# Performance work log

Hardware: AMD Instinct MI355X
Metric: run time of the kernel (lower is better)

## Reference

```python
import jax, jax.numpy as jnp
import numpy as np

N = 50000
E = 800000
IN_C = 256
NHID = 32
HEADS = 4
OUT_C = 64
HID = NHID * HEADS  # 128
SLOPE = 0.2


def setup_inputs() -> dict:
    key = jax.random.key(0)
    ks = jax.random.split(key, 16)
    s = lambda *d: 1.0 / np.sqrt(d[0])
    inp = {
        "x": jax.random.normal(ks[0], (N, IN_C), dtype=jnp.float32),
        "edge_index": jax.random.randint(ks[1], (2, E), 0, N, dtype=jnp.int64),
        # conv1: GATConv(IN_C, NHID, heads=HEADS, concat=True)
        "W1": jax.random.normal(ks[2], (IN_C, HEADS * NHID), dtype=jnp.float32) * s(IN_C),
        "att_src1": jax.random.normal(ks[3], (HEADS, NHID), dtype=jnp.float32) * s(NHID),
        "att_dst1": jax.random.normal(ks[4], (HEADS, NHID), dtype=jnp.float32) * s(NHID),
        "b1": jnp.zeros((HEADS * NHID,), dtype=jnp.float32),
        # conv2: GATConv(HID, OUT_C, heads=1, concat=False)
        "W2": jax.random.normal(ks[5], (HID, OUT_C), dtype=jnp.float32) * s(HID),
        "att_src2": jax.random.normal(ks[6], (1, OUT_C), dtype=jnp.float32) * s(OUT_C),
        "att_dst2": jax.random.normal(ks[7], (1, OUT_C), dtype=jnp.float32) * s(OUT_C),
        "b2": jnp.zeros((OUT_C,), dtype=jnp.float32),
        # res1: Linear(IN_C, HID)
        "res1_w": jax.random.normal(ks[8], (IN_C, HID), dtype=jnp.float32) * s(IN_C),
        "res1_b": jnp.zeros((HID,), dtype=jnp.float32),
        # fc: Linear(HID, OUT_C)
        "fc_w": jax.random.normal(ks[9], (HID, OUT_C), dtype=jnp.float32) * s(HID),
        "fc_b": jnp.zeros((OUT_C,), dtype=jnp.float32),
    }
    return inp


def leaky_relu(x, slope=SLOPE):
    return jnp.where(x >= 0, x, slope * x)


def gat_conv(x, edge_index, W, att_src, att_dst, bias, heads, out_c, concat):
    """PyG GATConv with default add_self_loops=True, negative_slope=0.2."""
    n = x.shape[0]
    loop = jnp.arange(n, dtype=edge_index.dtype)
    src = jnp.concatenate([edge_index[0], loop])  # [E+N]
    dst = jnp.concatenate([edge_index[1], loop])
    h = (x @ W).reshape(n, heads, out_c)          # [N,H,C]
    a_src = (h * att_src[None]).sum(-1)           # [N,H]
    a_dst = (h * att_dst[None]).sum(-1)
    alpha = leaky_relu(a_src[src] + a_dst[dst])   # [E+N,H]
    # segment softmax over destination nodes (every node has a self loop)
    amax = jax.ops.segment_max(alpha, dst, num_segments=n)
    expa = jnp.exp(alpha - amax[dst])
    denom = jax.ops.segment_sum(expa, dst, num_segments=n)
    alpha = expa / (denom[dst] + 1e-16)
    msg = alpha[:, :, None] * h[src]              # [E+N,H,C] irregular gather
    out = jax.ops.segment_sum(msg, dst, num_segments=n)  # scatter-add
    if concat:
        out = out.reshape(n, heads * out_c)
    else:
        out = out.mean(axis=1)
    return out + bias


def reference(x, edge_index, W1, att_src1, att_dst1, b1, W2, att_src2, att_dst2, b2,
              res1_w, res1_b, fc_w, fc_b):
    x_res = x @ res1_w + res1_b
    h = gat_conv(x, edge_index, W1, att_src1, att_dst1, b1, HEADS, NHID, True) + x_res
    h_res = h @ fc_w + fc_b
    h = leaky_relu(h)
    z = gat_conv(h, edge_index, W2, att_src2, att_dst2, b2, 1, OUT_C, False) + h_res
    z = leaky_relu(z)
    return z
```

## Files before the change

### kernel.cpp

```cpp
#include <hip/hip_runtime.h>

typedef __attribute__((ext_vector_type(8))) short short8;
typedef __attribute__((ext_vector_type(4))) float f32x4;

constexpr int BCAP = 4096;

__device__ __forceinline__ ushort rne_bf16(float f) {
  uint u = __float_as_uint(f);
  uint r = (u + 0x7FFFu + ((u >> 16) & 1u)) >> 16;
  return (ushort)r;
}
__device__ __forceinline__ float bf16_lo(uint pair) { return __uint_as_float(pair << 16); }
__device__ __forceinline__ float bf16_hi(uint pair) { return __uint_as_float(pair & 0xffff0000u); }
__device__ __forceinline__ float bf1(ushort v) { return __uint_as_float((uint)v << 16); }
__device__ __forceinline__ float lrelu(float a) { return a >= 0.f ? a : 0.2f * a; }

__device__ __forceinline__ uint lrelu_pair(uint pair) {
  float lo = lrelu(bf16_lo(pair));
  float hi = lrelu(bf16_hi(pair));
  return (uint)rne_bf16(lo) | ((uint)rne_bf16(hi) << 16);
}
__device__ __forceinline__ float4 lrelu_bf8(float4 v) {
  uint4 u = *(uint4*)&v;
  u.x = lrelu_pair(u.x); u.y = lrelu_pair(u.y);
  u.z = lrelu_pair(u.z); u.w = lrelu_pair(u.w);
  return *(float4*)&u;
}

__global__ __launch_bounds__(256) void prep_all_k(
    const float* __restrict__ x, ushort* __restrict__ x_bf, long nitems,
    const int* __restrict__ ei, int E, int nEB,
    int* __restrict__ bcnt, uint2* __restrict__ tmp, int nbuck,
    const float* __restrict__ W1, const float* __restrict__ res1_w,
    const float* __restrict__ fc_w, const float* __restrict__ W2,
    ushort* __restrict__ Wt1, ushort* __restrict__ fcT, ushort* __restrict__ W2T)
{
  __shared__ int lcnt[400];
  __shared__ int gbase[400];
  const int tid = threadIdx.x, bid = blockIdx.x;
  const long gstride = (long)gridDim.x * 256;
  const long g0 = (long)bid * 256 + tid;

  for (long it = g0; it < nitems; it += gstride) {
    long i = it * 8;
    float4 a = *(const float4*)&x[i];
    float4 b = *(const float4*)&x[i + 4];
    ushort o[8] = {rne_bf16(a.x), rne_bf16(a.y), rne_bf16(a.z), rne_bf16(a.w),
                   rne_bf16(b.x), rne_bf16(b.y), rne_bf16(b.z), rne_bf16(b.w)};
    *(uint4*)&x_bf[i] = *(const uint4*)o;
  }

  if (bid < nEB) {
    for (int i = tid; i < nbuck; i += 256) lcnt[i] = 0;
    __syncthreads();
    const int ebase = bid * 4096;
    int srcs[16], dsts[16], rk[16];
#pragma unroll
    for (int i = 0; i < 16; ++i) {
      int e = ebase + i * 256 + tid;
      if (e < E) {
        srcs[i] = ei[e];
        dsts[i] = ei[E + e];
        rk[i] = atomicAdd(&lcnt[dsts[i] >> 7], 1);
      } else dsts[i] = -1;
    }
    __syncthreads();
    for (int b = tid; b < nbuck; b += 256)
      gbase[b] = lcnt[b] ? atomicAdd(&bcnt[b], lcnt[b]) : 0;
    __syncthreads();
#pragma unroll
    for (int i = 0; i < 16; ++i) {
      if (dsts[i] >= 0) {
        int b = dsts[i] >> 7;
        tmp[(size_t)b * BCAP + gbase[b] + rk[i]] = make_uint2((uint)srcs[i], (uint)dsts[i]);
      }
    }
  }

  for (long gi = g0; gi < 81920; gi += gstride) {
    const float* src; ushort* dst; int K, NO; long local;
    if (gi < 32768)            { src = W1;     dst = Wt1;          K = 256; NO = 128; local = gi; }
    else if (gi < 65536)       { src = res1_w; dst = Wt1 + 32768;  K = 256; NO = 128; local = gi - 32768; }
    else if (gi < 65536+8192)  { src = fc_w;   dst = fcT;          K = 128; NO = 64;  local = gi - 65536; }
    else                       { src = W2;     dst = W2T;          K = 128; NO = 64;  local = gi - 65536 - 8192; }
    int n = (int)(local / K), k = (int)(local % K);
    dst[local] = rne_bf16(src[(size_t)k * NO + n]);
  }
}

__global__ __launch_bounds__(512) void scan_buckets_k(const int* __restrict__ bcnt,
                                                      int* __restrict__ bbase,
                                                      int* __restrict__ offp,
                                                      int nbuck, int N) {
  __shared__ int sh[512];
  int tid = threadIdx.x;
  int v = (tid < nbuck) ? bcnt[tid] : 0;
  sh[tid] = v;
  __syncthreads();
  for (int o = 1; o < 512; o <<= 1) {
    int t = (tid >= o) ? sh[tid - o] : 0;
    __syncthreads();
    sh[tid] += t;
    __syncthreads();
  }
  if (tid < nbuck) bbase[tid] = sh[tid] - v;
  if (tid == nbuck - 1) { bbase[nbuck] = sh[tid]; offp[N] = sh[tid]; }
}

__global__ __launch_bounds__(512) void gemm1_k(
    const ushort* __restrict__ x_bf, const ushort* __restrict__ Wt1,
    const float* __restrict__ res1_b,
    const float* __restrict__ att_s1, const float* __restrict__ att_d1,
    ushort* __restrict__ h1bf, ushort* __restrict__ xresbf,
    float* __restrict__ a_s, float* __restrict__ a_d,
    const uint2* __restrict__ tmp, const int* __restrict__ bcnt,
    const int* __restrict__ bbase, int* __restrict__ offp,
    int* __restrict__ csr, int nbuck, int M)
{
  constexpr int LDA = 72;
  __shared__ ushort smem[64 * LDA + 256 * LDA];
  const int bid = blockIdx.x, tid = threadIdx.x;
  ushort* As = smem;
  ushort* Bs = smem + 64 * LDA;
  const int w = tid >> 6, l = tid & 63;
  const int wr = w >> 2, wc = w & 3;
  const int l15 = l & 15, lg = l >> 4;
  const int row0 = bid * 64;
  const int srow = tid >> 3, sch = tid & 7;

  int gra = row0 + srow; if (gra >= M) gra = M - 1;
  const ushort* Ap = x_bf + (size_t)gra * 256 + sch * 8;
  const ushort* Bp = Wt1 + (size_t)srow * 256 + sch * 8;

  f32x4 acc[2][4] = {};
  float4 raC, rbC0, rbC1, rbC2, rbC3, raN, rbN0, rbN1, rbN2, rbN3;
  raC  = *(const float4*)(Ap);
  rbC0 = *(const float4*)(Bp);
  rbC1 = *(const float4*)(Bp + 64 * 256);
  rbC2 = *(const float4*)(Bp + 128 * 256);
  rbC3 = *(const float4*)(Bp + 192 * 256);

#pragma unroll
  for (int kt = 0; kt < 4; ++kt) {
    __syncthreads();
    *(float4*)&As[srow * LDA + sch * 8] = raC;
    *(float4*)&Bs[(0 * 64 + srow) * LDA + sch * 8] = rbC0;
    *(float4*)&Bs[(1 * 64 + srow) * LDA + sch * 8] = rbC1;
    *(float4*)&Bs[(2 * 64 + srow) * LDA + sch * 8] = rbC2;
    *(float4*)&Bs[(3 * 64 + srow) * LDA + sch * 8] = rbC3;
    __syncthreads();
    if (kt < 3) {
      int k1 = (kt + 1) * 64;
      raN  = *(const float4*)(Ap + k1);
      rbN0 = *(const float4*)(Bp + k1);
      rbN1 = *(const float4*)(Bp + 64 * 256 + k1);
      rbN2 = *(const float4*)(Bp + 128 * 256 + k1);
      rbN3 = *(const float4*)(Bp + 192 * 256 + k1);
    }
    short8 aF[2][2], bF[4][2];
#pragma unroll
    for (int m = 0; m < 2; ++m)
#pragma unroll
      for (int kk = 0; kk < 2; ++kk)
        aF[m][kk] = *(const short8*)&As[(wr * 32 + m * 16 + l15) * LDA + kk * 32 + lg * 8];
#pragma unroll
    for (int n = 0; n < 4; ++n)
#pragma unroll
      for (int kk = 0; kk < 2; ++kk)
        bF[n][kk] = *(const short8*)&Bs[(wc * 64 + n * 16 + l15) * LDA + kk * 32 + lg * 8];
#pragma unroll
    for (int m = 0; m < 2; ++m)
#pragma unroll
      for (int n = 0; n < 4; ++n)
#pragma unroll
        for (int kk = 0; kk < 2; ++kk)
          acc[m][n] = __builtin_amdgcn_mfma_f32_16x16x32_bf16(aF[m][kk], bF[n][kk], acc[m][n], 0, 0, 0);
    raC = raN; rbC0 = rbN0; rbC1 = rbN1; rbC2 = rbN2; rbC3 = rbN3;
  }
  __syncthreads();

  ushort* Cs = smem;
#pragma unroll
  for (int m = 0; m < 2; ++m)
#pragma unroll
    for (int n = 0; n < 4; ++n)
#pragma unroll
      for (int j = 0; j < 4; ++j) {
        int rl = wr * 32 + m * 16 + lg * 4 + j;
        int col = wc * 64 + n * 16 + l15;
        float v = acc[m][n][j] + (col >= 128 ? res1_b[col - 128] : 0.f);
        Cs[rl * 256 + col] = rne_bf16(v);
      }
  __syncthreads();

  {
    int r = tid >> 3, s = tid & 7, h = s >> 1;
    int gr = row0 + r;
    float ps = 0.f, pd = 0.f;
#pragma unroll
    for (int i = 0; i < 16; ++i) {
      int col = s * 16 + i;
      float v = bf1(Cs[r * 256 + col]);
      ps += v * att_s1[h * 32 + (col & 31)];
      pd += v * att_d1[h * 32 + (col & 31)];
    }
    ps += __shfl_xor(ps, 1, 64);
    pd += __shfl_xor(pd, 1, 64);
    if (!(s & 1) && gr < M) { a_s[gr * 4 + h] = ps; a_d[gr * 4 + h] = pd; }
  }

#pragma unroll
  for (int idx = tid; idx < 2048; idx += 512) {
    int row = idx >> 5, c16 = idx & 31;
    int gr = row0 + row;
    if (gr < M) {
      uint4 v = *(const uint4*)&Cs[row * 256 + c16 * 8];
      if (c16 < 16) *(uint4*)&h1bf[(size_t)gr * 128 + c16 * 8] = v;
      else          *(uint4*)&xresbf[(size_t)gr * 128 + (c16 - 16) * 8] = v;
    }
  }

  if (bid < nbuck) {
    __syncthreads();
    int* lcnt = (int*)smem;
    int* excl = lcnt + 128;
    const int vbase = bid * 128;
    const int nloc = ((vbase + 128 < M) ? 128 : M - vbase);
    const int cntb = bcnt[bid];
    const int bbase0 = bbase[bid];
    const uint2* bt = tmp + (size_t)bid * BCAP;
    if (tid < 128) lcnt[tid] = 0;
    __syncthreads();
    for (int e = tid; e < cntb; e += 512)
      atomicAdd(&lcnt[(int)bt[e].y - vbase], 1);
    __syncthreads();
    if (tid < 128) {
      int v = lcnt[tid];
      int sc = v;
#pragma unroll
      for (int o = 1; o < 64; o <<= 1) {
        int t = __shfl_up(sc, o, 64);
        if ((tid & 63) >= o) sc += t;
      }
      excl[tid] = sc - v;
    }
    __syncthreads();
    if (tid >= 64 && tid < 128) excl[tid] += excl[63] + lcnt[63];
    __syncthreads();
    if (tid < nloc) offp[vbase + tid] = bbase0 + excl[tid];
    if (tid < 128) lcnt[tid] = 0;
    __syncthreads();
    for (int e = tid; e < cntb; e += 512) {
      uint2 t = bt[e];
      int li = (int)t.y - vbase;
      int r = atomicAdd(&lcnt[li], 1);
      csr[bbase0 + excl[li] + r] = (int)t.x;
    }
  }
}

__global__ __launch_bounds__(512) void gemm2_k(
    const ushort* __restrict__ hpre,
    const ushort* __restrict__ fcT,
    const float* __restrict__ fc_b,
    const float* __restrict__ att_s2, const float* __restrict__ att_d2,
    ushort* __restrict__ hresb, ushort* __restrict__ h2bf,
    float* __restrict__ a_s, float* __restrict__ a_d, int M)
{
  constexpr int LDA = 72;
  __shared__ ushort smem[64 * LDA + 64 * LDA];
  const int tid = threadIdx.x, y = blockIdx.y;
  const ushort* B = fcT + (size_t)y * 64 * 128;
  ushort* out = y ? h2bf : hresb;
  const int row0 = blockIdx.x * 64;
  ushort* As = smem;
  ushort* Bs = smem + 64 * LDA;
  const int w = tid >> 6, l = tid & 63;
  const int wr = w >> 1, wc = w & 1;
  const int l15 = l & 15, lg = l >> 4;
  const int srow = tid >> 3, sch = tid & 7;

  int gra = row0 + srow; if (gra >= M) gra = M - 1;
  const ushort* Ap = hpre + (size_t)gra * 128 + sch * 8;
  const ushort* Bp = B + (size_t)srow * 128 + sch * 8;

  f32x4 acc[2] = {};
  float4 raC = *(const float4*)(Ap);
  float4 rbC = *(const float4*)(Bp);
  if (y) raC = lrelu_bf8(raC);
  float4 raN, rbN;

#pragma unroll
  for (int kt = 0; kt < 2; ++kt) {
    __syncthreads();
    *(float4*)&As[srow * LDA + sch * 8] = raC;
    *(float4*)&Bs[srow * LDA + sch * 8] = rbC;
    __syncthreads();
    if (kt < 1) {
      raN = *(const float4*)(Ap + 64);
      rbN = *(const float4*)(Bp + 64);
      if (y) raN = lrelu_bf8(raN);
    }

    short8 aF[2], bF[2][2];
#pragma unroll
    for (int kk = 0; kk < 2; ++kk)
      aF[kk] = *(const short8*)&As[(wr * 16 + l15) * LDA + kk * 32 + lg * 8];
#pragma unroll
    for (int n = 0; n < 2; ++n)
#pragma unroll
      for (int kk = 0; kk < 2; ++kk)
        bF[n][kk] = *(const short8*)&Bs[(wc * 32 + n * 16 + l15) * LDA + kk * 32 + lg * 8];
#pragma unroll
    for (int n = 0; n < 2; ++n)
#pragma unroll
      for (int kk = 0; kk < 2; ++kk)
        acc[n] = __builtin_amdgcn_mfma_f32_16x16x32_bf16(aF[kk], bF[n][kk], acc[n], 0, 0, 0);
    raC = raN; rbC = rbN;
  }
  __syncthreads();

  ushort* Cs = smem;
#pragma unroll
  for (int n = 0; n < 2; ++n)
#pragma unroll
    for (int j = 0; j < 4; ++j) {
      int rl = wr * 16 + lg * 4 + j;
      int col = wc * 32 + n * 16 + l15;
      float v = acc[n][j] + (y == 0 ? fc_b[col] : 0.f);
      Cs[rl * 64 + col] = rne_bf16(v);
    }
  __syncthreads();

  if (y == 1) {
    int r = tid >> 3, s = tid & 7;
    int gr = row0 + r;
    float ps = 0.f, pd = 0.f;
#pragma unroll
    for (int i = 0; i < 8; ++i) {
      int col = s * 8 + i;
      float v = bf1(Cs[r * 64 + col]);
      ps += v * att_s2[col];
      pd += v * att_d2[col];
    }
    ps += __shfl_xor(ps, 1, 64); pd += __shfl_xor(pd, 1, 64);
    ps += __shfl_xor(ps, 2, 64); pd += __shfl_xor(pd, 2, 64);
    ps += __shfl_xor(ps, 4, 64); pd += __shfl_xor(pd, 4, 64);
    if (s == 0 && gr < M) { a_s[gr] = ps; a_d[gr] = pd; }
  }

  {
    int row = tid >> 3, c16 = tid & 7;
    int gr = row0 + row;
    if (gr < M)
      *(uint4*)&out[(size_t)gr * 64 + c16 * 8] = *(const uint4*)&Cs[row * 64 + c16 * 8];
  }
}

__global__ __launch_bounds__(256) void aggr1_k(const uint* __restrict__ h1u,
                                               const uint* __restrict__ xresu,
                                               const float* __restrict__ a_s,
                                               const float* __restrict__ a_d,
                                               const int* __restrict__ off,
                                               const int* __restrict__ csr,
                                               const float* __restrict__ b1,
                                               uint* __restrict__ hpre_bf, int n) {
  int w = threadIdx.x >> 6, l = threadIdx.x & 63;
  int d = blockIdx.x * 4 + w;
  if (d >= n) return;
  int h = l >> 4, c = l * 2;
  int le = l & 15, hb = l & 48;
  float adh = a_d[d * 4 + h];
  float ws = __expf(lrelu(a_s[d * 4 + h] + adh));
  uint pd = h1u[(size_t)d * 64 + l];
  float lsum = ws, accx = ws * bf16_lo(pd), accy = ws * bf16_hi(pd);

  int s0 = off[d], s1 = off[d + 1];
  for (int p = s0; p < s1; p += 16) {
    int jp = p + le;
    bool valid = jp < s1;
    int jc = valid ? jp : s1 - 1;
    int idxv = csr[jc];
    float wv = valid ? __expf(lrelu(a_s[idxv * 4 + h] + adh)) : 0.f;
    float wi[16]; int sv[16];
#pragma unroll
    for (int i = 0; i < 16; ++i) {
      wi[i] = __shfl(wv, hb + i, 64);
      sv[i] = __shfl(idxv, i, 64);
    }
#pragma unroll
    for (int i = 0; i < 16; ++i) {
      uint q = h1u[(size_t)sv[i] * 64 + l];
      lsum += wi[i];
      accx += wi[i] * bf16_lo(q);
      accy += wi[i] * bf16_hi(q);
    }
  }
  float inv = 1.f / (lsum + 1e-16f);
  uint xr = xresu[(size_t)d * 64 + l];
  float vx = accx * inv + b1[c] + bf16_lo(xr);
  float vy = accy * inv + b1[c + 1] + bf16_hi(xr);
  hpre_bf[(size_t)d * 64 + l] = (uint)rne_bf16(vx) | ((uint)rne_bf16(vy) << 16);
}

__global__ __launch_bounds__(256) void aggr2_k(const ushort* __restrict__ h2b,
                                               const ushort* __restrict__ hresb,
                                               const float* __restrict__ a_s,
                                               const float* __restrict__ a_d,
                                               const int* __restrict__ off,
                                               const int* __restrict__ csr,
                                               const float* __restrict__ b2,
                                               float* __restrict__ out, int n) {
  int w = threadIdx.x >> 6, l = threadIdx.x & 63;
  int d = blockIdx.x * 4 + w;
  if (d >= n) return;
  int le = l & 15;
  float adh = a_d[d];
  float ws = __expf(lrelu(a_s[d] + adh));
  float lsum = ws;
  float acc = ws * bf1(h2b[(size_t)d * 64 + l]);

  int s0 = off[d], s1 = off[d + 1];
  for (int p = s0; p < s1; p += 16) {
    int jp = p + le;
    bool valid = jp < s1;
    int jc = valid ? jp : s1 - 1;
    int idxv = csr[jc];
    float wv = valid ? __expf(lrelu(a_s[idxv] + adh)) : 0.f;
    float wi[16]; int sv[16];
#pragma unroll
    for (int i = 0; i < 16; ++i) {
      wi[i] = __shfl(wv, i, 64);
      sv[i] = __shfl(idxv, i, 64);
    }
#pragma unroll
    for (int i = 0; i < 16; ++i) {
      float fv = bf1(h2b[(size_t)sv[i] * 64 + l]);
      lsum += wi[i];
      acc += wi[i] * fv;
    }
  }
  float inv = 1.f / (lsum + 1e-16f);
  float z = acc * inv + b2[l] + bf1(hresb[(size_t)d * 64 + l]);
  out[(size_t)d * 64 + l] = lrelu(z);
}

extern "C" void kernel_launch(void* const* d_in, const int* in_sizes, int n_in,
                              void* d_out, int out_size, void* d_ws, size_t ws_size,
                              hipStream_t stream) {
  const float* x        = (const float*)d_in[0];
  const int*   ei       = (const int*)d_in[1];
  const float* W1       = (const float*)d_in[2];
  const float* att_src1 = (const float*)d_in[3];
  const float* att_dst1 = (const float*)d_in[4];
  const float* b1       = (const float*)d_in[5];
  const float* W2       = (const float*)d_in[6];
  const float* att_src2 = (const float*)d_in[7];
  const float* att_dst2 = (const float*)d_in[8];
  const float* b2       = (const float*)d_in[9];
  const float* res1_w   = (const float*)d_in[10];
  const float* res1_b   = (const float*)d_in[11];
  const float* fc_w     = (const float*)d_in[12];
  const float* fc_b     = (const float*)d_in[13];
  float* out = (float*)d_out;

  const int N = in_sizes[0] / 256;
  const int E = in_sizes[1] / 2;
  const int nbuck = (N + 127) / 128;
  const int nEB = (E + 4095) / 4096;

  ushort* x_bf   = (ushort*)d_ws;
  ushort* h1bf   = x_bf + (size_t)N * 256;
  ushort* xresbf = h1bf + (size_t)N * 128;
  float*  as1    = (float*)(xresbf + (size_t)N * 128);
  float*  ad1    = as1 + (size_t)N * 4;
  ushort* Wt1    = (ushort*)(ad1 + (size_t)N * 4);
  ushort* fcT    = Wt1 + 256 * 256;
  ushort* W2T    = fcT + 64 * 128;
  int* offp      = (int*)(W2T + 64 * 128);
  int* csr       = offp + N + 1;
  int* bcnt      = csr + E;
  int* bbase     = bcnt + 512;
  uint2* tmp     = (uint2*)(((uintptr_t)(bbase + 520) + 7) & ~(uintptr_t)7);
  uint*   hpre_bf = (uint*)x_bf;
  ushort* h2bf    = h1bf;
  ushort* hresb   = xresbf;
  float*  as2 = as1, *ad2 = ad1;

  const int ngemm = (N + 63) / 64;

  hipMemsetAsync(bcnt, 0, 512 * 4, stream);
  prep_all_k<<<2048, 256, 0, stream>>>(x, x_bf, (long)N * 256 / 8, ei, E, nEB,
                                       bcnt, tmp, nbuck,
                                       W1, res1_w, fc_w, W2, Wt1, fcT, W2T);
  scan_buckets_k<<<1, 512, 0, stream>>>(bcnt, bbase, offp, nbuck, N);

  gemm1_k<<<ngemm, 512, 0, stream>>>(x_bf, Wt1, res1_b, att_src1, att_dst1,
                                     h1bf, xresbf, as1, ad1,
                                     tmp, bcnt, bbase, offp, csr, nbuck, N);

  aggr1_k<<<(N + 3) / 4, 256, 0, stream>>>((const uint*)h1bf, (const uint*)xresbf, as1, ad1,
                                           offp, csr, b1, hpre_bf, N);

  gemm2_k<<<dim3(ngemm, 2), 512, 0, stream>>>(
      (const ushort*)hpre_bf, fcT, fc_b,
      att_src2, att_dst2, hresb, h2bf, as2, ad2, N);

  aggr2_k<<<(N + 3) / 4, 256, 0, stream>>>(h2bf, hresb, as2, ad2, offp, csr, b2, out, N);
}
```

Before: 156.8 us.

## Fuse x bf16 conversion into gemm1 load and split aggregation tail loops

Drops the separate pass in prep_all_k that converted x from fp32 to bf16 into a workspace buffer. gemm1_k now reads fp32 x directly and packs it to bf16 on its way into shared memory, which removes a full write and re-read of the converted copy. prep_all_k is launched with only as many blocks as the edge bucketing needs, and the intermediate activation gets its own workspace buffer. Both aggregation kernels now run full 16-edge chunks without validity checks and handle the remainder in a separate tail loop. In exchange, gemm1 reads twice as many bytes for its A operand and spends extra ALU work on the conversion.

```diff
diff --git a/kernel.cpp b/kernel.cpp
--- a/kernel.cpp
+++ b/kernel.cpp
@@ -26,9 +26,16 @@
   u.z = lrelu_pair(u.z); u.w = lrelu_pair(u.w);
   return *(float4*)&u;
 }
+__device__ __forceinline__ float4 pack_bf8(float4 a, float4 b) {
+  uint u0 = (uint)rne_bf16(a.x) | ((uint)rne_bf16(a.y) << 16);
+  uint u1 = (uint)rne_bf16(a.z) | ((uint)rne_bf16(a.w) << 16);
+  uint u2 = (uint)rne_bf16(b.x) | ((uint)rne_bf16(b.y) << 16);
+  uint u3 = (uint)rne_bf16(b.z) | ((uint)rne_bf16(b.w) << 16);
+  uint4 r; r.x = u0; r.y = u1; r.z = u2; r.w = u3;
+  return *(float4*)&r;
+}
 
 __global__ __launch_bounds__(256) void prep_all_k(
-    const float* __restrict__ x, ushort* __restrict__ x_bf, long nitems,
     const int* __restrict__ ei, int E, int nEB,
     int* __restrict__ bcnt, uint2* __restrict__ tmp, int nbuck,
     const float* __restrict__ W1, const float* __restrict__ res1_w,
@@ -41,15 +48,6 @@
   const long gstride = (long)gridDim.x * 256;
   const long g0 = (long)bid * 256 + tid;
 
-  for (long it = g0; it < nitems; it += gstride) {
-    long i = it * 8;
-    float4 a = *(const float4*)&x[i];
-    float4 b = *(const float4*)&x[i + 4];
-    ushort o[8] = {rne_bf16(a.x), rne_bf16(a.y), rne_bf16(a.z), rne_bf16(a.w),
-                   rne_bf16(b.x), rne_bf16(b.y), rne_bf16(b.z), rne_bf16(b.w)};
-    *(uint4*)&x_bf[i] = *(const uint4*)o;
-  }
-
   if (bid < nEB) {
     for (int i = tid; i < nbuck; i += 256) lcnt[i] = 0;
     __syncthreads();
@@ -108,7 +106,7 @@
 }
 
 __global__ __launch_bounds__(512) void gemm1_k(
-    const ushort* __restrict__ x_bf, const ushort* __restrict__ Wt1,
+    const float* __restrict__ x, const ushort* __restrict__ Wt1,
     const float* __restrict__ res1_b,
     const float* __restrict__ att_s1, const float* __restrict__ att_d1,
     ushort* __restrict__ h1bf, ushort* __restrict__ xresbf,
@@ -129,12 +127,14 @@
   const int srow = tid >> 3, sch = tid & 7;
 
   int gra = row0 + srow; if (gra >= M) gra = M - 1;
-  const ushort* Ap = x_bf + (size_t)gra * 256 + sch * 8;
-  const ushort* Bp = Wt1 + (size_t)srow * 256 + sch * 8;
+  const float*  Apf = x + (size_t)gra * 256 + sch * 8;
+  const ushort* Bp  = Wt1 + (size_t)srow * 256 + sch * 8;
 
   f32x4 acc[2][4] = {};
-  float4 raC, rbC0, rbC1, rbC2, rbC3, raN, rbN0, rbN1, rbN2, rbN3;
-  raC  = *(const float4*)(Ap);
+  float4 raCa, raCb, rbC0, rbC1, rbC2, rbC3;
+  float4 raNa, raNb, rbN0, rbN1, rbN2, rbN3;
+  raCa = *(const float4*)(Apf);
+  raCb = *(const float4*)(Apf + 4);
   rbC0 = *(const float4*)(Bp);
   rbC1 = *(const float4*)(Bp + 64 * 256);
   rbC2 = *(const float4*)(Bp + 128 * 256);
@@ -143,7 +143,7 @@
 #pragma unroll
   for (int kt = 0; kt < 4; ++kt) {
     __syncthreads();
-    *(float4*)&As[srow * LDA + sch * 8] = raC;
+    *(float4*)&As[srow * LDA + sch * 8] = pack_bf8(raCa, raCb);
     *(float4*)&Bs[(0 * 64 + srow) * LDA + sch * 8] = rbC0;
     *(float4*)&Bs[(1 * 64 + srow) * LDA + sch * 8] = rbC1;
     *(float4*)&Bs[(2 * 64 + srow) * LDA + sch * 8] = rbC2;
@@ -151,7 +151,8 @@
     __syncthreads();
     if (kt < 3) {
       int k1 = (kt + 1) * 64;
-      raN  = *(const float4*)(Ap + k1);
+      raNa = *(const float4*)(Apf + k1);
+      raNb = *(const float4*)(Apf + k1 + 4);
       rbN0 = *(const float4*)(Bp + k1);
       rbN1 = *(const float4*)(Bp + 64 * 256 + k1);
       rbN2 = *(const float4*)(Bp + 128 * 256 + k1);
@@ -175,7 +176,8 @@
 #pragma unroll
         for (int kk = 0; kk < 2; ++kk)
           acc[m][n] = __builtin_amdgcn_mfma_f32_16x16x32_bf16(aF[m][kk], bF[n][kk], acc[m][n], 0, 0, 0);
-    raC = raN; rbC0 = rbN0; rbC1 = rbN1; rbC2 = rbN2; rbC3 = rbN3;
+    raCa = raNa; raCb = raNb;
+    rbC0 = rbN0; rbC1 = rbN1; rbC2 = rbN2; rbC3 = rbN3;
   }
   __syncthreads();
 
@@ -364,7 +366,7 @@
                                                const int* __restrict__ off,
                                                const int* __restrict__ csr,
                                                const float* __restrict__ b1,
-                                               uint* __restrict__ hpre_bf, int n) {
+                                               uint* __restrict__ hpreu, int n) {
   int w = threadIdx.x >> 6, l = threadIdx.x & 63;
   int d = blockIdx.x * 4 + w;
   if (d >= n) return;
@@ -376,31 +378,48 @@
   float lsum = ws, accx = ws * bf16_lo(pd), accy = ws * bf16_hi(pd);
 
   int s0 = off[d], s1 = off[d + 1];
-  for (int p = s0; p < s1; p += 16) {
+  int p = s0;
+  for (; p + 16 <= s1; p += 16) {
+    int idxv = csr[p + le];
+    float wv = __expf(lrelu(a_s[idxv * 4 + h] + adh));
+    float wi[16]; int sv[16];
+#pragma unroll
+    for (int i = 0; i < 16; ++i) {
+      wi[i] = __shfl(wv, hb + i, 64);
+      sv[i] = __shfl(idxv, i, 64);
+    }
+#pragma unroll
+    for (int i = 0; i < 16; ++i) {
+      uint q = h1u[(size_t)sv[i] * 64 + l];
+      lsum += wi[i];
+      accx += wi[i] * bf16_lo(q);
+      accy += wi[i] * bf16_hi(q);
+    }
+  }
+  if (p < s1) {
+    int rem = s1 - p;
     int jp = p + le;
     bool valid = jp < s1;
     int jc = valid ? jp : s1 - 1;
     int idxv = csr[jc];
     float wv = valid ? __expf(lrelu(a_s[idxv * 4 + h] + adh)) : 0.f;
-    float wi[16]; int sv[16];
-#pragma unroll
-    for (int i = 0; i < 16; ++i) {
-      wi[i] = __shfl(wv, hb + i, 64);
-      sv[i] = __shfl(idxv, i, 64);
-    }
-#pragma unroll
-    for (int i = 0; i < 16; ++i) {
-      uint q = h1u[(size_t)sv[i] * 64 + l];
-      lsum += wi[i];
-      accx += wi[i] * bf16_lo(q);
-      accy += wi[i] * bf16_hi(q);
+    for (int i = 0; i < rem; i += 4) {
+#pragma unroll
+      for (int j = 0; j < 4; ++j) {
+        float wib = __shfl(wv, hb + i + j, 64);
+        int svb = __shfl(idxv, i + j, 64);
+        uint q = h1u[(size_t)svb * 64 + l];
+        lsum += wib;
+        accx += wib * bf16_lo(q);
+        accy += wib * bf16_hi(q);
+      }
     }
   }
   float inv = 1.f / (lsum + 1e-16f);
   uint xr = xresu[(size_t)d * 64 + l];
   float vx = accx * inv + b1[c] + bf16_lo(xr);
   float vy = accy * inv + b1[c + 1] + bf16_hi(xr);
-  hpre_bf[(size_t)d * 64 + l] = (uint)rne_bf16(vx) | ((uint)rne_bf16(vy) << 16);
+  hpreu[(size_t)d * 64 + l] = (uint)rne_bf16(vx) | ((uint)rne_bf16(vy) << 16);
 }
 
 __global__ __launch_bounds__(256) void aggr2_k(const ushort* __restrict__ h2b,
@@ -421,23 +440,39 @@
   float acc = ws * bf1(h2b[(size_t)d * 64 + l]);
 
   int s0 = off[d], s1 = off[d + 1];
-  for (int p = s0; p < s1; p += 16) {
+  int p = s0;
+  for (; p + 16 <= s1; p += 16) {
+    int idxv = csr[p + le];
+    float wv = __expf(lrelu(a_s[idxv] + adh));
+    float wi[16]; int sv[16];
+#pragma unroll
+    for (int i = 0; i < 16; ++i) {
+      wi[i] = __shfl(wv, i, 64);
+      sv[i] = __shfl(idxv, i, 64);
+    }
+#pragma unroll
+    for (int i = 0; i < 16; ++i) {
+      float fv = bf1(h2b[(size_t)sv[i] * 64 + l]);
+      lsum += wi[i];
+      acc += wi[i] * fv;
+    }
+  }
+  if (p < s1) {
+    int rem = s1 - p;
     int jp = p + le;
     bool valid = jp < s1;
     int jc = valid ? jp : s1 - 1;
     int idxv = csr[jc];
     float wv = valid ? __expf(lrelu(a_s[idxv] + adh)) : 0.f;
-    float wi[16]; int sv[16];
-#pragma unroll
-    for (int i = 0; i < 16; ++i) {
-      wi[i] = __shfl(wv, i, 64);
-      sv[i] = __shfl(idxv, i, 64);
-    }
-#pragma unroll
-    for (int i = 0; i < 16; ++i) {
-      float fv = bf1(h2b[(size_t)sv[i] * 64 + l]);
-      lsum += wi[i];
-      acc += wi[i] * fv;
+    for (int i = 0; i < rem; i += 4) {
+#pragma unroll
+      for (int j = 0; j < 4; ++j) {
+        float wib = __shfl(wv, i + j, 64);
+        int svb = __shfl(idxv, i + j, 64);
+        float fv = bf1(h2b[(size_t)svb * 64 + l]);
+        lsum += wib;
+        acc += wib * fv;
+      }
     }
   }
   float inv = 1.f / (lsum + 1e-16f);
@@ -469,10 +504,10 @@
   const int nbuck = (N + 127) / 128;
   const int nEB = (E + 4095) / 4096;
 
-  ushort* x_bf   = (ushort*)d_ws;
-  ushort* h1bf   = x_bf + (size_t)N * 256;
+  ushort* h1bf   = (ushort*)d_ws;
   ushort* xresbf = h1bf + (size_t)N * 128;
-  float*  as1    = (float*)(xresbf + (size_t)N * 128);
+  uint*   hpreu  = (uint*)(xresbf + (size_t)N * 128);
+  float*  as1    = (float*)(hpreu + (size_t)N * 64);
   float*  ad1    = as1 + (size_t)N * 4;
   ushort* Wt1    = (ushort*)(ad1 + (size_t)N * 4);
   ushort* fcT    = Wt1 + 256 * 256;
@@ -482,28 +517,26 @@
   int* bcnt      = csr + E;
   int* bbase     = bcnt + 512;
   uint2* tmp     = (uint2*)(((uintptr_t)(bbase + 520) + 7) & ~(uintptr_t)7);
-  uint*   hpre_bf = (uint*)x_bf;
-  ushort* h2bf    = h1bf;
-  ushort* hresb   = xresbf;
+  ushort* h2bf   = h1bf;
+  ushort* hresb  = xresbf;
   float*  as2 = as1, *ad2 = ad1;
 
   const int ngemm = (N + 63) / 64;
 
   hipMemsetAsync(bcnt, 0, 512 * 4, stream);
-  prep_all_k<<<2048, 256, 0, stream>>>(x, x_bf, (long)N * 256 / 8, ei, E, nEB,
-                                       bcnt, tmp, nbuck,
-                                       W1, res1_w, fc_w, W2, Wt1, fcT, W2T);
+  prep_all_k<<<nEB, 256, 0, stream>>>(ei, E, nEB, bcnt, tmp, nbuck,
+                                      W1, res1_w, fc_w, W2, Wt1, fcT, W2T);
   scan_buckets_k<<<1, 512, 0, stream>>>(bcnt, bbase, offp, nbuck, N);
 
-  gemm1_k<<<ngemm, 512, 0, stream>>>(x_bf, Wt1, res1_b, att_src1, att_dst1,
+  gemm1_k<<<ngemm, 512, 0, stream>>>(x, Wt1, res1_b, att_src1, att_dst1,
                                      h1bf, xresbf, as1, ad1,
                                      tmp, bcnt, bbase, offp, csr, nbuck, N);
 
   aggr1_k<<<(N + 3) / 4, 256, 0, stream>>>((const uint*)h1bf, (const uint*)xresbf, as1, ad1,
-                                           offp, csr, b1, hpre_bf, N);
+                                           offp, csr, b1, hpreu, N);
 
   gemm2_k<<<dim3(ngemm, 2), 512, 0, stream>>>(
-      (const ushort*)hpre_bf, fcT, fc_b,
+      (const ushort*)hpreu, fcT, fc_b,
       att_src2, att_dst2, hresb, h2bf, as2, ad2, N);
 
   aggr2_k<<<(N + 3) / 4, 256, 0, stream>>>(h2bf, hresb, as2, ad2, offp, csr, b2, out, N);
```

Result: faster. 153.7 us (-2.0%).
